# Optimization experiments

Measured on AMD Instinct MI355X. Metric: run time of the kernel, lower is better.

Reference implementation:

```python
import jax, jax.numpy as jnp
import numpy as np

# Module config (from init_kwargs): causal=False, window_size=(256,256), window_type=0,
# softmax_scale=None -> 1/sqrt(D), dropout=0 (eval mode).
WINDOW_LEFT, WINDOW_RIGHT = 256, 256


def _window_mask(Sq, Sk, causal, use_window_mask):
    """Boolean [Sq, Sk] visibility mask, FA2 semantics (right-aligned offset)."""
    qi = jnp.arange(Sq)[:, None]
    kj = jnp.arange(Sk)[None, :]
    offset = Sk - Sq
    if causal:
        return kj <= qi + offset  # window (-1, 0)
    if use_window_mask:
        m = jnp.ones((Sq, Sk), dtype=bool)
        if WINDOW_LEFT >= 0:
            m = m & (kj >= qi + offset - WINDOW_LEFT)
        if WINDOW_RIGHT >= 0:
            m = m & (kj <= qi + offset + WINDOW_RIGHT)
        return m
    return None  # full attention


def setup_inputs() -> dict:
    key = jax.random.key(0)
    kq, kkv = jax.random.split(key)
    B, Sq, Sk, H, D = 2, 2048, 2048, 16, 64
    q = jax.random.normal(kq, (B, Sq, H, D), dtype=jnp.float32)
    kv = jax.random.normal(kkv, (B, Sk, 2, H, D), dtype=jnp.float32)
    return {"q": q, "kv": kv, "causal": 0, "use_window_mask": 1, "return_attn_probs": 0}


def reference(q, kv, causal, use_window_mask, return_attn_probs):
    # q: (B, Sq, H, D); kv: (B, Sk, 2, H, D)
    B, Sq, H, D = q.shape
    Sk = kv.shape[1]
    k = kv[:, :, 0]  # (B, Sk, H, D)
    v = kv[:, :, 1]
    scale = 1.0 / (D ** 0.5)
    scores = jnp.einsum('bqhd,bkhd->bhqk', q, k) * scale  # (B, H, Sq, Sk)
    mask = _window_mask(Sq, Sk, bool(causal), bool(use_window_mask))
    if mask is not None:
        scores = jnp.where(mask[None, None], scores, jnp.finfo(scores.dtype).min)
    probs = jax.nn.softmax(scores, axis=-1)
    out = jnp.einsum('bhqk,bkhd->bqhd', probs, v)  # (B, Sq, H, D)
    return out
```

## Files before the change

kernel.cpp:

```cpp
#include <hip/hip_runtime.h>
#include <hip/hip_bf16.h>

#define B_    2
#define SQ_   2048
#define SK_   2048
#define NH_   16
#define DH_   64
#define WIN_  256
#define NEG_  -30000.0f

typedef __bf16 bf16_t;
typedef bf16_t bf16x8 __attribute__((ext_vector_type(8)));
typedef bf16_t bf16x4 __attribute__((ext_vector_type(4)));
typedef float  f32x4  __attribute__((ext_vector_type(4)));

#define KSTRIDE 72
#define VSTRIDE 72
#define PSTRIDE 72

__global__ __launch_bounds__(512, 4)
void fa_fwd(const float* __restrict__ qg, const float* __restrict__ kvg,
            float* __restrict__ outg) {
  const int tid  = threadIdx.x;
  const int wid  = tid >> 6;
  const int lane = tid & 63;
  const int quad = lane >> 4;
  const int li   = lane & 15;

  const int bid = blockIdx.x;
  const int qb  = bid >> 5;
  const int bh  = bid & 31;
  const int b   = bh >> 4;
  const int h   = bh & 15;

  const int q0b = qb * 128;
  const int q0  = q0b + wid * 16;

  __shared__ __align__(16) bf16_t sK [2][64 * KSTRIDE];
  __shared__ __align__(16) bf16_t sVT[2][64 * VSTRIDE];
  __shared__ __align__(16) bf16_t sP [8][16 * PSTRIDE];
  bf16_t* pl = sP[wid];

  const float qscale = 0.125f * 1.44269504088896340736f;
  const float* qrow = qg + ((size_t)((b * SQ_ + q0 + li) * NH_ + h)) * DH_;
  bf16x8 qfrag[2];
#pragma unroll
  for (int c = 0; c < 2; ++c) {
    f32x4 a0 = *(const f32x4*)(qrow + c * 32 + quad * 8);
    f32x4 a1 = *(const f32x4*)(qrow + c * 32 + quad * 8 + 4);
#pragma unroll
    for (int i = 0; i < 4; ++i) {
      qfrag[c][i]     = (bf16_t)(a0[i] * qscale);
      qfrag[c][i + 4] = (bf16_t)(a1[i] * qscale);
    }
  }

  f32x4 oacc[4];
#pragma unroll
  for (int t = 0; t < 4; ++t) { f32x4 z = {0.f, 0.f, 0.f, 0.f}; oacc[t] = z; }
  float m = NEG_, l = 0.f;

  int klo = q0b - WIN_; if (klo < 0) klo = 0;
  int khi = q0b + 127 + WIN_ + 1; if (khi > SK_) khi = SK_;

  const float* kbase = kvg + (size_t)b * SK_ * 2 * NH_ * DH_ + (size_t)h * DH_;
  const float* vbase = kbase + NH_ * DH_;
  const size_t krow_stride = 2 * NH_ * DH_;

  const int skey = tid >> 3;
  const int sd0  = (tid & 7) * 8;
  const int vcol = skey ^ (((sd0 >> 3) & 7) << 3);

  f32x4 ka[2], va[2];
  {
    const float* kr = kbase + (size_t)(klo + skey) * krow_stride + sd0;
    const float* vr = vbase + (size_t)(klo + skey) * krow_stride + sd0;
    ka[0] = *(const f32x4*)kr;       ka[1] = *(const f32x4*)(kr + 4);
    va[0] = *(const f32x4*)vr;       va[1] = *(const f32x4*)(vr + 4);
  }
  {
    bf16x8 w;
#pragma unroll
    for (int i = 0; i < 4; ++i) { w[i] = (bf16_t)ka[0][i]; w[i + 4] = (bf16_t)ka[1][i]; }
    *(bf16x8*)(&sK[0][skey * KSTRIDE + sd0]) = w;
#pragma unroll
    for (int i = 0; i < 4; ++i) {
      sVT[0][(sd0 + i)     * VSTRIDE + vcol] = (bf16_t)va[0][i];
      sVT[0][(sd0 + 4 + i) * VSTRIDE + vcol] = (bf16_t)va[1][i];
    }
  }
  __syncthreads();

  int buf = 0;
  for (int kk = klo; kk < khi; kk += 64) {
    const bool nxt = (kk + 64 < khi);
    if (nxt) {
      const float* kr = kbase + (size_t)(kk + 64 + skey) * krow_stride + sd0;
      const float* vr = vbase + (size_t)(kk + 64 + skey) * krow_stride + sd0;
      ka[0] = *(const f32x4*)kr;       ka[1] = *(const f32x4*)(kr + 4);
      va[0] = *(const f32x4*)vr;       va[1] = *(const f32x4*)(vr + 4);
    }

    if (kk + 63 >= q0 - WIN_ && kk <= q0 + 15 + WIN_) {
      f32x4 sc[4];
#pragma unroll
      for (int s = 0; s < 4; ++s) {
        bf16x8 kf0 = *(const bf16x8*)(&sK[buf][(s * 16 + li) * KSTRIDE + quad * 8]);
        bf16x8 kf1 = *(const bf16x8*)(&sK[buf][(s * 16 + li) * KSTRIDE + 32 + quad * 8]);
        f32x4 acc = {0.f, 0.f, 0.f, 0.f};
        acc = __builtin_amdgcn_mfma_f32_16x16x32_bf16(kf0, qfrag[0], acc, 0, 0, 0);
        acc = __builtin_amdgcn_mfma_f32_16x16x32_bf16(kf1, qfrag[1], acc, 0, 0, 0);
        sc[s] = acc;
      }
      if (kk < q0 - 241 || kk > q0 + 193) {
        const int qa = q0 + li;
#pragma unroll
        for (int s = 0; s < 4; ++s)
#pragma unroll
          for (int r = 0; r < 4; ++r) {
            int key = kk + s * 16 + quad * 4 + r;
            unsigned dd = (unsigned)(key - qa + WIN_);
            if (dd > 2u * WIN_) sc[s][r] = NEG_;
          }
      }
      float tmax = NEG_;
#pragma unroll
      for (int s = 0; s < 4; ++s)
        tmax = fmaxf(tmax, fmaxf(fmaxf(sc[s][0], sc[s][1]), fmaxf(sc[s][2], sc[s][3])));
      tmax = fmaxf(tmax, __shfl_xor(tmax, 16));
      tmax = fmaxf(tmax, __shfl_xor(tmax, 32));
      float mnew  = fmaxf(m, tmax);
      float alpha = exp2f(m - mnew);
      float psum = 0.f;
#pragma unroll
      for (int s = 0; s < 4; ++s) {
        bf16x4 pk;
#pragma unroll
        for (int r = 0; r < 4; ++r) {
          float p = exp2f(sc[s][r] - mnew);
          psum += p;
          pk[r] = (bf16_t)p;
        }
        *(bf16x4*)(&pl[li * PSTRIDE + s * 16 + quad * 4]) = pk;
      }
      psum += __shfl_xor(psum, 16);
      psum += __shfl_xor(psum, 32);
      l = l * alpha + psum;
      m = mnew;

      asm volatile("s_waitcnt lgkmcnt(0)" ::: "memory");

      float al[4];
#pragma unroll
      for (int r = 0; r < 4; ++r) al[r] = __shfl(alpha, quad * 4 + r);
#pragma unroll
      for (int t = 0; t < 4; ++t) {
        oacc[t][0] *= al[0]; oacc[t][1] *= al[1];
        oacc[t][2] *= al[2]; oacc[t][3] *= al[3];
      }
#pragma unroll
      for (int kc = 0; kc < 2; ++kc) {
        bf16x8 pf = *(const bf16x8*)(&pl[li * PSTRIDE + kc * 32 + quad * 8]);
#pragma unroll
        for (int t = 0; t < 4; ++t) {
          const int d = 16 * t + li;
          const int c = ((2 * t + (li >> 3)) & 7) << 3;
          bf16x8 vf = *(const bf16x8*)(&sVT[buf][d * VSTRIDE + ((kc * 32 + quad * 8) ^ c)]);
          oacc[t] = __builtin_amdgcn_mfma_f32_16x16x32_bf16(pf, vf, oacc[t], 0, 0, 0);
        }
      }
    }

    if (nxt) {
      bf16x8 w;
#pragma unroll
      for (int i = 0; i < 4; ++i) { w[i] = (bf16_t)ka[0][i]; w[i + 4] = (bf16_t)ka[1][i]; }
      *(bf16x8*)(&sK[buf ^ 1][skey * KSTRIDE + sd0]) = w;
#pragma unroll
      for (int i = 0; i < 4; ++i) {
        sVT[buf ^ 1][(sd0 + i)     * VSTRIDE + vcol] = (bf16_t)va[0][i];
        sVT[buf ^ 1][(sd0 + 4 + i) * VSTRIDE + vcol] = (bf16_t)va[1][i];
      }
    }
    __syncthreads();
    buf ^= 1;
  }

  float rl[4];
#pragma unroll
  for (int r = 0; r < 4; ++r) {
    float lv = __shfl(l, quad * 4 + r);
    rl[r] = 1.0f / lv;
  }
  float* orow = outg + ((size_t)((b * SQ_ + q0) * NH_ + h)) * DH_;
#pragma unroll
  for (int t = 0; t < 4; ++t)
#pragma unroll
    for (int r = 0; r < 4; ++r)
      orow[(size_t)(quad * 4 + r) * (NH_ * DH_) + 16 * t + li] = oacc[t][r] * rl[r];
}

extern "C" void kernel_launch(void* const* d_in, const int* in_sizes, int n_in,
                              void* d_out, int out_size, void* d_ws, size_t ws_size,
                              hipStream_t stream) {
  (void)in_sizes; (void)n_in; (void)out_size; (void)d_ws; (void)ws_size;
  const float* q  = (const float*)d_in[0];
  const float* kv = (const float*)d_in[1];
  float* out = (float*)d_out;
  dim3 grid(B_ * NH_ * (SQ_ / 128));
  fa_fwd<<<grid, 512, 0, stream>>>(q, kv, out);
}
```

Before: 114.1 us.

## Feed P from registers via 16x16x16 MFMA and defer softmax rescaling

The P tile is no longer round-tripped through shared memory. Its exponentials stay in registers and go straight into 16x16x16 bf16 MFMAs, whose input layout matches the score accumulator layout. This drops the LDS writes, the waitcnt and the reads of P. The change also skips the running-max update and the output rescale when no row's tile max exceeds the current max by more than 8 (in log2 units), which saves exp and multiply work. The cost is twice as many MFMA instructions at half the K depth, and possibly larger fp32 intermediates when rescaling is deferred.

```diff
diff --git a/kernel.cpp b/kernel.cpp
--- a/kernel.cpp
+++ b/kernel.cpp
@@ -13,10 +13,17 @@
 typedef bf16_t bf16x8 __attribute__((ext_vector_type(8)));
 typedef bf16_t bf16x4 __attribute__((ext_vector_type(4)));
 typedef float  f32x4  __attribute__((ext_vector_type(4)));
+typedef short  s16x4  __attribute__((ext_vector_type(4)));
 
 #define KSTRIDE 72
 #define VSTRIDE 72
 #define PSTRIDE 72
+
+#if defined(__has_builtin)
+#if __has_builtin(__builtin_amdgcn_mfma_f32_16x16x16bf16_1k)
+#define HAVE_MFMA16 1
+#endif
+#endif
 
 __global__ __launch_bounds__(512, 4)
 void fa_fwd(const float* __restrict__ qg, const float* __restrict__ kvg,
@@ -38,8 +45,10 @@
 
   __shared__ __align__(16) bf16_t sK [2][64 * KSTRIDE];
   __shared__ __align__(16) bf16_t sVT[2][64 * VSTRIDE];
+#ifndef HAVE_MFMA16
   __shared__ __align__(16) bf16_t sP [8][16 * PSTRIDE];
   bf16_t* pl = sP[wid];
+#endif
 
   const float qscale = 0.125f * 1.44269504088896340736f;
   const float* qrow = qg + ((size_t)((b * SQ_ + q0 + li) * NH_ + h)) * DH_;
@@ -129,9 +138,24 @@
         tmax = fmaxf(tmax, fmaxf(fmaxf(sc[s][0], sc[s][1]), fmaxf(sc[s][2], sc[s][3])));
       tmax = fmaxf(tmax, __shfl_xor(tmax, 16));
       tmax = fmaxf(tmax, __shfl_xor(tmax, 32));
-      float mnew  = fmaxf(m, tmax);
-      float alpha = exp2f(m - mnew);
+
+      const bool defer = (__all(tmax <= m + 8.0f) != 0);
+      const float mnew = defer ? m : fmaxf(m, tmax);
+
       float psum = 0.f;
+#ifdef HAVE_MFMA16
+      bf16x4 pa[4];
+#pragma unroll
+      for (int s = 0; s < 4; ++s) {
+        float p0 = exp2f(sc[s][0] - mnew);
+        float p1 = exp2f(sc[s][1] - mnew);
+        float p2 = exp2f(sc[s][2] - mnew);
+        float p3 = exp2f(sc[s][3] - mnew);
+        psum += (p0 + p1) + (p2 + p3);
+        pa[s][0] = (bf16_t)p0; pa[s][1] = (bf16_t)p1;
+        pa[s][2] = (bf16_t)p2; pa[s][3] = (bf16_t)p3;
+      }
+#else
 #pragma unroll
       for (int s = 0; s < 4; ++s) {
         bf16x4 pk;
@@ -143,21 +167,40 @@
         }
         *(bf16x4*)(&pl[li * PSTRIDE + s * 16 + quad * 4]) = pk;
       }
+#endif
       psum += __shfl_xor(psum, 16);
       psum += __shfl_xor(psum, 32);
-      l = l * alpha + psum;
-      m = mnew;
-
+
+      if (!defer) {
+        const float alpha = exp2f(m - mnew);
+        float al[4];
+#pragma unroll
+        for (int r = 0; r < 4; ++r) al[r] = __shfl(alpha, quad * 4 + r);
+#pragma unroll
+        for (int t = 0; t < 4; ++t) {
+          oacc[t][0] *= al[0]; oacc[t][1] *= al[1];
+          oacc[t][2] *= al[2]; oacc[t][3] *= al[3];
+        }
+        l = l * alpha + psum;
+        m = mnew;
+      } else {
+        l += psum;
+      }
+
+#ifdef HAVE_MFMA16
+#pragma unroll
+      for (int s = 0; s < 4; ++s) {
+        const s16x4 pas = __builtin_bit_cast(s16x4, pa[s]);
+#pragma unroll
+        for (int t = 0; t < 4; ++t) {
+          const int d  = 16 * t + li;
+          const int c8 = ((2 * t + (li >> 3)) & 7) << 3;
+          s16x4 vb = *(const s16x4*)(&sVT[buf][d * VSTRIDE + ((s * 16 + quad * 4) ^ c8)]);
+          oacc[t] = __builtin_amdgcn_mfma_f32_16x16x16bf16_1k(pas, vb, oacc[t], 0, 0, 0);
+        }
+      }
+#else
       asm volatile("s_waitcnt lgkmcnt(0)" ::: "memory");
-
-      float al[4];
-#pragma unroll
-      for (int r = 0; r < 4; ++r) al[r] = __shfl(alpha, quad * 4 + r);
-#pragma unroll
-      for (int t = 0; t < 4; ++t) {
-        oacc[t][0] *= al[0]; oacc[t][1] *= al[1];
-        oacc[t][2] *= al[2]; oacc[t][3] *= al[3];
-      }
 #pragma unroll
       for (int kc = 0; kc < 2; ++kc) {
         bf16x8 pf = *(const bf16x8*)(&pl[li * PSTRIDE + kc * 32 + quad * 8]);
@@ -169,6 +212,7 @@
           oacc[t] = __builtin_amdgcn_mfma_f32_16x16x32_bf16(pf, vf, oacc[t], 0, 0, 0);
         }
       }
+#endif
     }
 
     if (nxt) {
```

After: 113.1 us. No clear change (-0.9%).
